# Kernel tuning notes

Measured on AMD Instinct MI355X. Metric: run time of the kernel, lower is better.

The kernel has to match this reference:

```python
import jax, jax.numpy as jnp
import numpy as np

# DualAttention dims
D_MODEL = 1024
H_SA = 8          # self-attention heads
H_RA = 8          # relational-attention heads
TOTAL_H = H_SA + H_RA
HEAD_DIM = D_MODEL // TOTAL_H   # 64
KEY_DIM = HEAD_DIM              # 64
N_REL = 8
REL_PROJ = HEAD_DIM * H_RA // N_REL  # 64
B, S = 2, 2048


def apply_rope(x, cos, sin):
    # x: [b, s, h, d]; cos/sin: [s, d//2]. Pairs are (0,1),(2,3),... as in
    # llama-style apply_rotary_emb (reshape(..., -1, 2).unbind(-1)).
    xr, xi = x[..., 0::2], x[..., 1::2]
    c = cos[None, :, None, :]
    s_ = sin[None, :, None, :]
    out = jnp.stack([xr * c - xi * s_, xr * s_ + xi * c], axis=-1)
    return out.reshape(x.shape)


def setup_inputs() -> dict:
    key = jax.random.key(0)
    ks = jax.random.split(key, 16)
    def w(k, shape):
        return jax.random.normal(k, shape, jnp.float32) * 0.02
    x = jax.random.normal(ks[0], (B, S, D_MODEL), jnp.float32)
    symbols = jax.random.normal(ks[1], (B, S, D_MODEL), jnp.float32)
    # real RoPE tables
    pos = np.arange(S, dtype=np.float32)[:, None]
    inv = 1.0 / (10000.0 ** (np.arange(0, KEY_DIM, 2, dtype=np.float32) / KEY_DIM))
    ang = pos * inv[None, :]
    freqs_cos = jnp.asarray(np.cos(ang), jnp.float32)
    freqs_sin = jnp.asarray(np.sin(ang), jnp.float32)
    return dict(
        x=x, symbols=symbols, freqs_cos=freqs_cos, freqs_sin=freqs_sin,
        # self-attention branch (torch Linear weights: [out, in])
        wq_sa=w(ks[2], (H_SA * KEY_DIM, D_MODEL)),
        wk_sa=w(ks[3], (H_SA * KEY_DIM, D_MODEL)),
        wv_sa=w(ks[4], (H_SA * HEAD_DIM, D_MODEL)),
        wo_sa=w(ks[5], (H_SA * HEAD_DIM, H_SA * HEAD_DIM)),
        # relational-attention branch
        wq_attn=w(ks[6], (H_RA * KEY_DIM, D_MODEL)),
        wk_attn=w(ks[7], (H_RA * KEY_DIM, D_MODEL)),
        wq_rel=w(ks[8], (N_REL * REL_PROJ, D_MODEL)),
        wk_rel=w(ks[9], (N_REL * REL_PROJ, D_MODEL)),
        wr=w(ks[10], (H_RA, HEAD_DIM, N_REL)),
        wv_ra=w(ks[11], (H_RA * HEAD_DIM, D_MODEL)),
        wo_ra=w(ks[12], (H_RA * HEAD_DIM, H_RA * HEAD_DIM)),
    )


def reference(x, symbols, freqs_cos, freqs_sin,
              wq_sa, wk_sa, wv_sa, wo_sa,
              wq_attn, wk_attn, wq_rel, wk_rel, wr, wv_ra, wo_ra):
    b, s, _ = x.shape
    attn_scale = 1.0 / np.sqrt(HEAD_DIM).astype(np.float32)
    rel_scale = 1.0 / np.sqrt(REL_PROJ).astype(np.float32)
    causal = jnp.tril(jnp.ones((s, s), dtype=bool))
    neg = jnp.finfo(x.dtype).min

    def heads(t, h, d):
        return t.reshape(b, s, h, d)

    # ---- self-attention branch (causal SDPA with RoPE) ----
    q = apply_rope(heads(x @ wq_sa.T, H_SA, KEY_DIM), freqs_cos, freqs_sin)
    k = apply_rope(heads(x @ wk_sa.T, H_SA, KEY_DIM), freqs_cos, freqs_sin)
    v = heads(x @ wv_sa.T, H_SA, HEAD_DIM)
    scores = jnp.einsum('bihd,bjhd->bhij', q, k) * attn_scale
    a = jax.nn.softmax(jnp.where(causal, scores, neg), axis=-1)
    sa_out = jnp.einsum('bhij,bjhd->bihd', a, v).reshape(b, s, H_SA * HEAD_DIM) @ wo_sa.T

    # ---- relational-attention branch ----
    # attention scores (softmax selection), with RoPE
    qa = apply_rope(heads(x @ wq_attn.T, H_RA, KEY_DIM), freqs_cos, freqs_sin)
    ka = apply_rope(heads(x @ wk_attn.T, H_RA, KEY_DIM), freqs_cos, freqs_sin)
    ra_scores = jnp.einsum('bihd,bjhd->bhij', qa, ka) * attn_scale
    alpha = jax.nn.softmax(jnp.where(causal, ra_scores, neg), axis=-1)
    # relations r(x_i, x_j) in R^{N_REL} (identity rel_activation)
    qr = heads(x @ wq_rel.T, N_REL, REL_PROJ)
    kr = heads(x @ wk_rel.T, N_REL, REL_PROJ)
    rel = jnp.einsum('birp,bjrp->brij', qr, kr) * rel_scale  # [b, R, i, j]
    # symbol values: wv applied to retrieved symbols
    sv = heads(symbols @ wv_ra.T, H_RA, HEAD_DIM)
    attended_sym = jnp.einsum('bhij,bjhd->bihd', alpha, sv)          # [b, i, h, d]
    attended_rel = jnp.einsum('bhij,brij->bihr', alpha, rel)         # [b, i, h, R]
    rel_out = jnp.einsum('bihr,hdr->bihd', attended_rel, wr)
    ra_out = (attended_sym + rel_out).reshape(b, s, H_RA * HEAD_DIM) @ wo_ra.T

    # DualAttention: concat branch outputs along feature dim -> [b, s, d_model]
    return jnp.concatenate([sa_out, ra_out], axis=-1)
```

## Files before the change

kernel.cpp:

```cpp
#include <hip/hip_runtime.h>

#define B_   2
#define S_   2048
#define H_   8
#define D_   64
#define DM_  1024
#define PJ_  512
#define NT_  32
#define NTRI 528
#define NCHK 80

typedef short bf16x8 __attribute__((ext_vector_type(8)));
typedef float f32x4 __attribute__((ext_vector_type(4)));

__device__ __forceinline__ float bf2f(unsigned int u) {
  return __uint_as_float(u << 16);
}
__device__ __forceinline__ unsigned short f2bf(float f) {
  unsigned int u = __float_as_uint(f);
  u += 0x7fffu + ((u >> 16) & 1u);
  return (unsigned short)(u >> 16);
}

__device__ __forceinline__ void glds16(const unsigned short* g, unsigned short* l) {
  __builtin_amdgcn_global_load_lds(
      (const __attribute__((address_space(1))) void*)g,
      (__attribute__((address_space(3))) void*)l, 16, 0, 0);
}

struct CvtJobs {
  const float*    src[12];
  unsigned short* dst[12];
  int             n4[12];
};

__global__ __launch_bounds__(256) void cvt_many(CvtJobs J) {
  const int j = blockIdx.y;
  const int i = blockIdx.x * 256 + threadIdx.x;
  if (i >= J.n4[j]) return;
  const float4 v = ((const float4*)J.src[j])[i];
  ushort4 o;
  o.x = f2bf(v.x); o.y = f2bf(v.y); o.z = f2bf(v.z); o.w = f2bf(v.w);
  ((ushort4*)J.dst[j])[i] = o;
}

__device__ __forceinline__
void gemm128_glds(const unsigned short* __restrict__ A, int m0,
                  const unsigned short* __restrict__ Wb,
                  unsigned short* __restrict__ Cb, int ldc, int KD,
                  unsigned short* As, unsigned short* Bs)
{
  const int tid = threadIdx.x;
  const int wv = tid >> 6, lane = tid & 63;
  const int r15 = lane & 15, quad = lane >> 4;
  const int wm = (wv >> 1) * 64, wn = (wv & 1) * 64;
  f32x4 acc[4][4];
#pragma unroll
  for (int i = 0; i < 4; ++i)
#pragma unroll
    for (int j = 0; j < 4; ++j) acc[i][j] = (f32x4){0.f, 0.f, 0.f, 0.f};

  const int srow = wv * 16 + (lane >> 2);
  const int scol = ((lane & 3) ^ ((lane >> 3) & 3)) * 8;
  const unsigned short* gaA0 = A + (size_t)(m0 + srow) * KD + scol;
  const unsigned short* gaA1 = gaA0 + (size_t)64 * KD;
  const unsigned short* gaB0 = Wb + (size_t)srow * KD + scol;
  const unsigned short* gaB1 = gaB0 + (size_t)64 * KD;
  unsigned short* ldsA0 = As + wv * 512;
  unsigned short* ldsA1 = As + 2048 + wv * 512;
  unsigned short* ldsB0 = Bs + wv * 512;
  unsigned short* ldsB1 = Bs + 2048 + wv * 512;
  const int rxor = (r15 >> 1) & 3;

  for (int kk = 0; kk < KD; kk += 32) {
    __syncthreads();
    glds16(gaA0 + kk, ldsA0);
    glds16(gaA1 + kk, ldsA1);
    glds16(gaB0 + kk, ldsB0);
    glds16(gaB1 + kk, ldsB1);
    __syncthreads();
    bf16x8 af[4], bf[4];
#pragma unroll
    for (int i = 0; i < 4; ++i)
      af[i] = *(const bf16x8*)(As + (wm + i * 16 + r15) * 32 + ((quad ^ rxor) << 3));
#pragma unroll
    for (int j = 0; j < 4; ++j)
      bf[j] = *(const bf16x8*)(Bs + (wn + j * 16 + r15) * 32 + ((quad ^ rxor) << 3));
#pragma unroll
    for (int i = 0; i < 4; ++i)
#pragma unroll
      for (int j = 0; j < 4; ++j)
        acc[i][j] = __builtin_amdgcn_mfma_f32_16x16x32_bf16(af[i], bf[j], acc[i][j], 0, 0, 0);
  }
#pragma unroll
  for (int i = 0; i < 4; ++i)
#pragma unroll
    for (int r = 0; r < 4; ++r) {
      unsigned short* cp = Cb + (size_t)(wm + i * 16 + quad * 4 + r) * ldc + wn + r15;
#pragma unroll
      for (int j = 0; j < 4; ++j) cp[j * 16] = f2bf(acc[i][j][r]);
    }
}

__global__ __launch_bounds__(256)
void proj_tiled(const unsigned short* __restrict__ XB,
                const unsigned short* __restrict__ SYB,
                const unsigned short* __restrict__ Wcat,
                unsigned short* __restrict__ Qbase,
                unsigned short* __restrict__ SV)
{
  __shared__ unsigned short As[128 * 32];
  __shared__ unsigned short Bs[128 * 32];
  const int m0 = blockIdx.x * 128;
  const int ny = blockIdx.y;
  const size_t NB = (size_t)B_ * S_ * PJ_;
  const unsigned short* A;
  const unsigned short* Wb;
  unsigned short* Cb;
  if (ny < 28) {
    const int n0 = ny * 128;
    A  = XB;
    Wb = Wcat + (size_t)n0 * DM_;
    Cb = Qbase + (size_t)(n0 >> 9) * NB + (size_t)m0 * PJ_ + (n0 & 511);
  } else {
    const int n0 = (ny - 28) * 128;
    A  = SYB;
    Wb = Wcat + (size_t)7 * PJ_ * DM_ + (size_t)n0 * DM_;
    Cb = SV + (size_t)m0 * PJ_ + n0;
  }
  gemm128_glds(A, m0, Wb, Cb, PJ_, DM_, As, Bs);
}

__global__ __launch_bounds__(256)
void out_tiled(const unsigned short* __restrict__ Asa,
               const unsigned short* __restrict__ Ara,
               const unsigned short* __restrict__ WOSA,
               const unsigned short* __restrict__ WORA,
               float* __restrict__ Out)
{
  __shared__ unsigned short As[128 * 40];
  __shared__ unsigned short Bs[64 * 40];
  const int m0 = blockIdx.x * 128;
  const int ny = blockIdx.y;
  const int n0 = (ny & 7) * 64;
  const unsigned short* A  = (ny < 8) ? Asa : Ara;
  const unsigned short* Wb = ((ny < 8) ? WOSA : WORA) + (size_t)n0 * PJ_;
  float* Cb = Out + (size_t)m0 * DM_ + ((ny < 8) ? 0 : 512) + n0;

  const int tid = threadIdx.x;
  const int wv = tid >> 6, lane = tid & 63;
  const int r15 = lane & 15, quad = lane >> 4;
  const int wm = wv * 32;
  f32x4 acc[2][4];
#pragma unroll
  for (int i = 0; i < 2; ++i)
#pragma unroll
    for (int j = 0; j < 4; ++j) acc[i][j] = (f32x4){0.f, 0.f, 0.f, 0.f};

  const int arow = tid >> 1, ac = (tid & 1) * 16;
  const int brow = tid >> 2, bc = (tid & 3) * 8;
  const unsigned short* ga = A + (size_t)(m0 + arow) * PJ_ + ac;
  const unsigned short* gb = Wb + (size_t)brow * PJ_ + bc;
  unsigned short* la = As + arow * 40 + ac;
  unsigned short* lb = Bs + brow * 40 + bc;

  for (int kk = 0; kk < PJ_; kk += 32) {
    __syncthreads();
    const uint4 a0 = *(const uint4*)(ga + kk);
    const uint4 a1 = *(const uint4*)(ga + kk + 8);
    const uint4 b0 = *(const uint4*)(gb + kk);
    *(uint4*)la       = a0;
    *(uint4*)(la + 8) = a1;
    *(uint4*)lb       = b0;
    __syncthreads();
    bf16x8 af[2], bf[4];
#pragma unroll
    for (int i = 0; i < 2; ++i)
      af[i] = *(const bf16x8*)(As + (wm + i * 16 + r15) * 40 + quad * 8);
#pragma unroll
    for (int j = 0; j < 4; ++j)
      bf[j] = *(const bf16x8*)(Bs + (j * 16 + r15) * 40 + quad * 8);
#pragma unroll
    for (int i = 0; i < 2; ++i)
#pragma unroll
      for (int j = 0; j < 4; ++j)
        acc[i][j] = __builtin_amdgcn_mfma_f32_16x16x32_bf16(af[i], bf[j], acc[i][j], 0, 0, 0);
  }
#pragma unroll
  for (int i = 0; i < 2; ++i)
#pragma unroll
    for (int r = 0; r < 4; ++r) {
      float* cp = Cb + (size_t)(wm + i * 16 + quad * 4 + r) * DM_ + r15;
#pragma unroll
      for (int j = 0; j < 4; ++j) cp[j * 16] = acc[i][j][r];
    }
}

__global__ __launch_bounds__(256)
void rel_rope(const unsigned short* __restrict__ QRg, const unsigned short* __restrict__ KRg,
              unsigned short* __restrict__ RelCF,
              unsigned short* __restrict__ Qp, unsigned short* __restrict__ Kp,
              unsigned short* __restrict__ QAp, unsigned short* __restrict__ KAp,
              const float* __restrict__ fcp, const float* __restrict__ fsp)
{
  __shared__ unsigned short As[128 * 72];
  __shared__ unsigned short Bs[128 * 72];
  const int t = blockIdx.x;
  int I = 0;
  while ((I + 1) * (I + 2) / 2 <= t) ++I;
  const int J = t - I * (I + 1) / 2;
  const int rr = blockIdx.y & 7, b = blockIdx.y >> 3;
  const int tid = threadIdx.x;
  const int wv = tid >> 6, lane = tid & 63;
  const int r15 = lane & 15, quad = lane >> 4;

  const int srow = tid >> 1, c32 = (tid & 1) * 32;
  const unsigned short* ga = QRg + (size_t)(b * S_ + I * 128 + srow) * PJ_ + rr * 64 + c32;
  const unsigned short* gb = KRg + (size_t)(b * S_ + J * 128 + srow) * PJ_ + rr * 64 + c32;
  unsigned short* la = As + srow * 72 + c32;
  unsigned short* lb = Bs + srow * 72 + c32;
#pragma unroll
  for (int q = 0; q < 4; ++q) {
    *(uint4*)(la + q * 8) = *(const uint4*)(ga + q * 8);
    *(uint4*)(lb + q * 8) = *(const uint4*)(gb + q * 8);
  }
  __syncthreads();

  const int wm = (wv >> 1) * 64, wn = (wv & 1) * 64;
  const int it64 = 2 * I + (wv >> 1), jt64 = 2 * J + (wv & 1);
  if (jt64 <= it64) {
    f32x4 acc[4][4];
#pragma unroll
    for (int a = 0; a < 4; ++a)
#pragma unroll
      for (int bq = 0; bq < 4; ++bq) acc[a][bq] = (f32x4){0.f, 0.f, 0.f, 0.f};
#pragma unroll
    for (int k0 = 0; k0 < 2; ++k0) {
      bf16x8 af[4], bf[4];
#pragma unroll
      for (int i = 0; i < 4; ++i)
        af[i] = *(const bf16x8*)(As + (wm + i * 16 + r15) * 72 + quad * 8 + k0 * 32);
#pragma unroll
      for (int j = 0; j < 4; ++j)
        bf[j] = *(const bf16x8*)(Bs + (wn + j * 16 + r15) * 72 + quad * 8 + k0 * 32);
#pragma unroll
      for (int a = 0; a < 4; ++a)
#pragma unroll
        for (int bq = 0; bq < 4; ++bq)
          acc[a][bq] = __builtin_amdgcn_mfma_f32_16x16x32_bf16(bf[a], af[bq], acc[a][bq], 0, 0, 0);
    }
    unsigned short* out = RelCF + ((size_t)(b * 8 + rr) * NTRI + (size_t)it64 * (it64 + 1) / 2 + jt64) * 4096;
#pragma unroll
    for (int bq = 0; bq < 4; ++bq) {
      unsigned short tmp[16];
#pragma unroll
      for (int a = 0; a < 4; ++a)
#pragma unroll
        for (int r = 0; r < 4; ++r)
          tmp[a * 4 + r] = f2bf(acc[a][bq][r] * 0.125f);
      unsigned short* op = out + (size_t)(bq * 64 + lane) * 16;
      *(uint4*)op       = *(const uint4*)tmp;
      *(uint4*)(op + 8) = *(const uint4*)(tmp + 8);
    }
  }

  const int bid = (int)blockIdx.y * 136 + (int)blockIdx.x;
  const int gt = bid * 256 + tid;
#pragma unroll
  for (int k = 0; k < 2; ++k) {
    const int i = gt * 2 + k;
    if (i >= 4 * 262144) continue;
    const int tn = i >> 18;
    const int r2 = i & 262143;
    unsigned short* P = (tn == 0) ? Qp : (tn == 1) ? Kp : (tn == 2) ? QAp : KAp;
    const int b2 = r2 >> 17;
    const int s2 = (r2 >> 6) & 2047;
    const int c8 = (r2 & 63) * 8;
    const int ci0 = (c8 & 63) >> 1;
    const size_t off2 = ((size_t)(b2 * S_ + s2)) * PJ_ + c8;
    uint4 v = *(const uint4*)(P + off2);
    unsigned int u[4] = {v.x, v.y, v.z, v.w};
    unsigned int o[4];
#pragma unroll
    for (int q = 0; q < 4; ++q) {
      const float xr = __uint_as_float(u[q] << 16);
      const float xi = __uint_as_float(u[q] & 0xffff0000u);
      const float cs = fcp[s2 * 32 + ci0 + q];
      const float sn = fsp[s2 * 32 + ci0 + q];
      const unsigned short lo = f2bf(xr * cs - xi * sn);
      const unsigned short hi = f2bf(xr * sn + xi * cs);
      o[q] = (unsigned int)lo | ((unsigned int)hi << 16);
    }
    uint4 ov; ov.x = o[0]; ov.y = o[1]; ov.z = o[2]; ov.w = o[3];
    *(uint4*)(P + off2) = ov;
  }
}

__global__ __launch_bounds__(256)
void flash_part(const unsigned short* __restrict__ Qsa, const unsigned short* __restrict__ Ksa,
                const unsigned short* __restrict__ Vsa,
                const unsigned short* __restrict__ Qra, const unsigned short* __restrict__ Kra,
                const unsigned short* __restrict__ SVra,
                const unsigned short* __restrict__ RelCF,
                unsigned short* __restrict__ PoP, float* __restrict__ lP,
                float* __restrict__ arpP)
{
  __shared__ unsigned short Ks[2][64][72];
  __shared__ unsigned short Vt[2][64][72];
  const int x = blockIdx.x;
  int it, c;
  if (x < 8)       { it = x;                    c = 0; }
  else if (x < 24) { it = 8 + ((x - 8) >> 1);   c = (x - 8) & 1; }
  else if (x < 48) { it = 16 + (x - 24) / 3;    c = (x - 24) % 3; }
  else             { it = 24 + ((x - 48) >> 2); c = (x - 48) & 3; }
  const int j0 = c * 8;
  const int jend = (j0 + 8 < it + 1) ? (j0 + 8) : (it + 1);
  const bool ra = (blockIdx.y >= 8);
  const int h = blockIdx.y & 7;
  const int b = blockIdx.z;
  const int chunkId = (b * 16 + (int)blockIdx.y) * NCHK + x;
  const unsigned short* Qg = ra ? Qra : Qsa;
  const unsigned short* Kg = ra ? Kra : Ksa;
  const unsigned short* Vg = ra ? SVra : Vsa;
  const int tid = threadIdx.x;
  const int wv = tid >> 6, lane = tid & 63;
  const int r15 = lane & 15, quad = lane >> 4;
  const size_t bh = (size_t)b * S_ * PJ_ + (size_t)h * D_;
  const size_t relStride = (size_t)NTRI * 4096;

  const int kr0 = tid >> 3, kc0 = (tid & 7) << 3;
  const int kr1 = (tid + 256) >> 3;
  const unsigned short* kgp = Kg + bh + kc0;
  const unsigned short* vgp = Vg + bh + (size_t)lane * PJ_ + wv * 8;
  const int kcol = ((lane >> 2) & 3) * 8 + ((lane >> 4) & 1) * 4 + (lane & 3) + (lane >> 5) * 32;

  const unsigned short* qp = Qg + bh + (size_t)(it * 64 + wv * 16 + r15) * PJ_ + quad * 8;
  const bf16x8 aq0 = *(const bf16x8*)qp;
  const bf16x8 aq1 = *(const bf16x8*)(qp + 32);

  f32x4 o_acc[4];
  float l_row = 0.f;
  float arp[8];
#pragma unroll
  for (int n = 0; n < 4; ++n) o_acc[n] = (f32x4){0.f, 0.f, 0.f, 0.f};
#pragma unroll
  for (int rr = 0; rr < 8; ++rr) arp[rr] = 0.f;
  const int il = wv * 16 + r15;
  const size_t relTileBase = (size_t)(b * 8) * NTRI * 4096
                           + (size_t)(it * (it + 1)) / 2 * 4096
                           + (size_t)(wv * 64 + lane) * 16;

  uint4 ka0, ka1, va0, va1;
  {
    const size_t jb = (size_t)j0 * 64 * PJ_;
    ka0 = *(const uint4*)(kgp + jb + (size_t)kr0 * PJ_);
    ka1 = *(const uint4*)(kgp + jb + (size_t)kr1 * PJ_);
    va0 = *(const uint4*)(vgp + jb);
    va1 = *(const uint4*)(vgp + jb + 32);
  }
  int p = 0;
  {
    *(uint4*)&Ks[0][kr0][kc0] = ka0;
    *(uint4*)&Ks[0][kr1][kc0] = ka1;
    unsigned short t8[8];
    *(uint4*)t8 = va0;
#pragma unroll
    for (int m = 0; m < 8; ++m) Vt[0][wv * 8 + m][kcol] = t8[m];
    *(uint4*)t8 = va1;
#pragma unroll
    for (int m = 0; m < 8; ++m) Vt[0][wv * 8 + 32 + m][kcol] = t8[m];
  }
  __syncthreads();

  for (int jt = j0; jt < jend; ++jt) {
    const bool more = (jt + 1 < jend);
    if (more) {
      const size_t jb = (size_t)(jt + 1) * 64 * PJ_;
      ka0 = *(const uint4*)(kgp + jb + (size_t)kr0 * PJ_);
      ka1 = *(const uint4*)(kgp + jb + (size_t)kr1 * PJ_);
      va0 = *(const uint4*)(vgp + jb);
      va1 = *(const uint4*)(vgp + jb + 32);
    }
    uint4 pre[8];
    const unsigned short* rtBase = RelCF + relTileBase + (size_t)jt * 4096;
    if (ra) {
      const unsigned short* rt = rtBase;
#pragma unroll
      for (int q = 0; q < 4; ++q) {
        pre[2 * q]     = *(const uint4*)rt;
        pre[2 * q + 1] = *(const uint4*)(rt + 8);
        rt += relStride;
      }
    }
    f32x4 s[4];
#pragma unroll
    for (int n = 0; n < 4; ++n) s[n] = (f32x4){0.f, 0.f, 0.f, 0.f};
#pragma unroll
    for (int k0 = 0; k0 < 2; ++k0) {
      const bf16x8 bq = k0 ? aq1 : aq0;
#pragma unroll
      for (int n = 0; n < 4; ++n) {
        const bf16x8 kf = *(const bf16x8*)&Ks[p][n * 16 + r15][quad * 8 + k0 * 32];
        s[n] = __builtin_amdgcn_mfma_f32_16x16x32_bf16(kf, bq, s[n], 0, 0, 0);
      }
    }
    if (jt == it) {
#pragma unroll
      for (int n = 0; n < 4; ++n)
#pragma unroll
        for (int r = 0; r < 4; ++r) {
          const bool ok = (n * 16 + quad * 4 + r <= il);
          s[n][r] = ok ? __expf(s[n][r] * 0.125f - 4.0f) : 0.f;
        }
    } else {
#pragma unroll
      for (int n = 0; n < 4; ++n)
#pragma unroll
        for (int r = 0; r < 4; ++r)
          s[n][r] = __expf(s[n][r] * 0.125f - 4.0f);
    }
    unsigned short pw[16];
#pragma unroll
    for (int jj = 0; jj < 8; ++jj) {
      pw[jj]     = f2bf(s[(jj >> 2)][jj & 3]);
      pw[8 + jj] = f2bf(s[2 + (jj >> 2)][jj & 3]);
    }
    const bf16x8 pa0 = *(const bf16x8*)pw;
    const bf16x8 pa1 = *(const bf16x8*)(pw + 8);
    {
      float ls = 0.f;
#pragma unroll
      for (int jj = 0; jj < 16; ++jj) ls += bf2f((unsigned int)pw[jj]);
      l_row += ls;
    }
#pragma unroll
    for (int k0 = 0; k0 < 2; ++k0) {
      const bf16x8 pf = k0 ? pa1 : pa0;
#pragma unroll
      for (int n = 0; n < 4; ++n) {
        const bf16x8 vf = *(const bf16x8*)&Vt[p][n * 16 + r15][quad * 8 + k0 * 32];
        o_acc[n] = __builtin_amdgcn_mfma_f32_16x16x32_bf16(pf, vf, o_acc[n], 0, 0, 0);
      }
    }
    if (ra) {
      const unsigned short* rt2 = rtBase + 4 * relStride;
#pragma unroll
      for (int rr = 0; rr < 8; ++rr) {
        unsigned int ru[8];
        if (rr < 4) {
          *(uint4*)ru       = pre[2 * rr];
          *(uint4*)(ru + 4) = pre[2 * rr + 1];
        } else {
          *(uint4*)ru       = *(const uint4*)rt2;
          *(uint4*)(ru + 4) = *(const uint4*)(rt2 + 8);
          rt2 += relStride;
        }
        float a = arp[rr];
#pragma unroll
        for (int n = 0; n < 4; ++n) {
          const unsigned int u0 = ru[2 * n], u1 = ru[2 * n + 1];
          a += s[n][0] * __uint_as_float(u0 << 16);
          a += s[n][1] * __uint_as_float(u0 & 0xffff0000u);
          a += s[n][2] * __uint_as_float(u1 << 16);
          a += s[n][3] * __uint_as_float(u1 & 0xffff0000u);
        }
        arp[rr] = a;
      }
    }
    if (more) {
      const int q = p ^ 1;
      *(uint4*)&Ks[q][kr0][kc0] = ka0;
      *(uint4*)&Ks[q][kr1][kc0] = ka1;
      unsigned short t8[8];
      *(uint4*)t8 = va0;
#pragma unroll
      for (int m = 0; m < 8; ++m) Vt[q][wv * 8 + m][kcol] = t8[m];
      *(uint4*)t8 = va1;
#pragma unroll
      for (int m = 0; m < 8; ++m) Vt[q][wv * 8 + 32 + m][kcol] = t8[m];
      __syncthreads();
      p = q;
    }
  }
  unsigned short* po = PoP + (size_t)chunkId * 4096;
#pragma unroll
  for (int n = 0; n < 4; ++n)
#pragma unroll
    for (int r = 0; r < 4; ++r)
      po[(wv * 16 + quad * 4 + r) * 64 + n * 16 + r15] = f2bf(o_acc[n][r]);
  l_row += __shfl_xor(l_row, 16);
  l_row += __shfl_xor(l_row, 32);
  if (lane < 16)
    lP[(size_t)chunkId * 64 + wv * 16 + lane] = l_row;
  if (ra) {
#pragma unroll
    for (int rr = 0; rr < 8; ++rr) {
      arp[rr] += __shfl_xor(arp[rr], 16);
      arp[rr] += __shfl_xor(arp[rr], 32);
    }
    if (lane < 16) {
      float* ap = arpP + (size_t)chunkId * 512 + (wv * 16 + lane) * 8;
#pragma unroll
      for (int rr = 0; rr < 8; ++rr) ap[rr] = arp[rr];
    }
  }
}

__global__ __launch_bounds__(256)
void flash_merge(const unsigned short* __restrict__ PoP, const float* __restrict__ lP,
                 const float* __restrict__ arpP, const float* __restrict__ wrF,
                 unsigned short* __restrict__ Osa, unsigned short* __restrict__ Ora)
{
  const int it = blockIdx.x;
  const int hh = blockIdx.y;
  const int b  = blockIdx.z;
  const bool ra = (hh >= 8);
  const int h = hh & 7;
  const int nc = it / 8 + 1;
  int cb;
  if (it < 8)       cb = it;
  else if (it < 16) cb = 8 + 2 * (it - 8);
  else if (it < 24) cb = 24 + 3 * (it - 16);
  else              cb = 48 + 4 * (it - 24);
  const int cid0 = (b * 16 + hh) * NCHK + cb;
  const int tid = threadIdx.x;
  const int row = tid >> 2;
  const int cg  = tid & 3;

  float L = 0.f;
  for (int c = 0; c < nc; ++c) L += lP[(size_t)(cid0 + c) * 64 + row];
  const float inv = 1.f / L;

  float o[16];
#pragma unroll
  for (int k = 0; k < 16; ++k) o[k] = 0.f;
  for (int c = 0; c < nc; ++c) {
    const unsigned short* pp = PoP + (size_t)(cid0 + c) * 4096 + row * 64 + cg * 16;
    unsigned int u[8];
    *(uint4*)u       = *(const uint4*)pp;
    *(uint4*)(u + 4) = *(const uint4*)(pp + 8);
#pragma unroll
    for (int q = 0; q < 8; ++q) {
      o[2 * q]     += __uint_as_float(u[q] << 16);
      o[2 * q + 1] += __uint_as_float(u[q] & 0xffff0000u);
    }
  }
  if (ra) {
    float A[8];
#pragma unroll
    for (int rr = 0; rr < 8; ++rr) A[rr] = 0.f;
    for (int c = 0; c < nc; ++c) {
      const float* ap = arpP + (size_t)(cid0 + c) * 512 + row * 8;
#pragma unroll
      for (int rr = 0; rr < 8; ++rr) A[rr] += ap[rr];
    }
#pragma unroll
    for (int k = 0; k < 16; ++k) {
      const float* wp = wrF + ((size_t)h * 64 + cg * 16 + k) * 8;
      float ro = 0.f;
#pragma unroll
      for (int rr = 0; rr < 8; ++rr) ro += A[rr] * wp[rr];
      o[k] += ro;
    }
  }
  const size_t bh = (size_t)b * S_ * PJ_ + (size_t)h * D_;
  unsigned short* op = (ra ? Ora : Osa) + bh + (size_t)(it * 64 + row) * PJ_ + cg * 16;
#pragma unroll
  for (int k = 0; k < 16; ++k) op[k] = f2bf(o[k] * inv);
}

extern "C" void kernel_launch(void* const* d_in, const int* in_sizes, int n_in,
                              void* d_out, int out_size, void* d_ws, size_t ws_size,
                              hipStream_t stream)
{
  (void)in_sizes; (void)n_in; (void)out_size; (void)ws_size;
  const float* x    = (const float*)d_in[0];
  const float* sym  = (const float*)d_in[1];
  const float* fc   = (const float*)d_in[2];
  const float* fs   = (const float*)d_in[3];
  const float* wqsa = (const float*)d_in[4];
  const float* wksa = (const float*)d_in[5];
  const float* wvsa = (const float*)d_in[6];
  const float* wosa = (const float*)d_in[7];
  const float* wqat = (const float*)d_in[8];
  const float* wkat = (const float*)d_in[9];
  const float* wqre = (const float*)d_in[10];
  const float* wkre = (const float*)d_in[11];
  const float* wr   = (const float*)d_in[12];
  const float* wvra = (const float*)d_in[13];
  const float* wora = (const float*)d_in[14];

  unsigned short* wsb = (unsigned short*)d_ws;
  const size_t NX = (size_t)B_ * S_ * DM_;
  const size_t NB = (size_t)B_ * S_ * PJ_;
  const size_t NW = (size_t)PJ_ * DM_;
  const size_t NO = (size_t)PJ_ * PJ_;
  const size_t NR = (size_t)B_ * 8 * NTRI * 4096;
  const size_t NCH = (size_t)B_ * 16 * NCHK;

  size_t off = 0;
  unsigned short* XB   = wsb + off; off += NX;
  unsigned short* SYB  = wsb + off; off += NX;
  unsigned short* WB[8];
  for (int i = 0; i < 8; ++i) { WB[i] = wsb + off; off += NW; }
  unsigned short* WOSA = wsb + off; off += NO;
  unsigned short* WORA = wsb + off; off += NO;
  unsigned short* Q    = wsb + off; off += NB;
  unsigned short* K    = wsb + off; off += NB;
  unsigned short* V    = wsb + off; off += NB;
  unsigned short* QA   = wsb + off; off += NB;
  unsigned short* KA   = wsb + off; off += NB;
  unsigned short* QR   = wsb + off; off += NB;
  unsigned short* KR   = wsb + off; off += NB;
  unsigned short* SV   = wsb + off; off += NB;
  unsigned short* Asa  = wsb + off; off += NB;
  unsigned short* Ara  = wsb + off; off += NB;
  unsigned short* RelCF = wsb + off; off += NR;
  unsigned short* PoP  = XB;
  float* lP   = (float*)(wsb + off); off += NCH * 64 * 2;
  float* arpP = (float*)(wsb + off); off += NCH * 512 * 2;

  CvtJobs cj;
  cj.src[0]  = x;    cj.dst[0]  = XB;    cj.n4[0]  = (int)(NX / 4);
  cj.src[1]  = sym;  cj.dst[1]  = SYB;   cj.n4[1]  = (int)(NX / 4);
  cj.src[2]  = wqsa; cj.dst[2]  = WB[0]; cj.n4[2]  = (int)(NW / 4);
  cj.src[3]  = wksa; cj.dst[3]  = WB[1]; cj.n4[3]  = (int)(NW / 4);
  cj.src[4]  = wvsa; cj.dst[4]  = WB[2]; cj.n4[4]  = (int)(NW / 4);
  cj.src[5]  = wqat; cj.dst[5]  = WB[3]; cj.n4[5]  = (int)(NW / 4);
  cj.src[6]  = wkat; cj.dst[6]  = WB[4]; cj.n4[6]  = (int)(NW / 4);
  cj.src[7]  = wqre; cj.dst[7]  = WB[5]; cj.n4[7]  = (int)(NW / 4);
  cj.src[8]  = wkre; cj.dst[8]  = WB[6]; cj.n4[8]  = (int)(NW / 4);
  cj.src[9]  = wvra; cj.dst[9]  = WB[7]; cj.n4[9]  = (int)(NW / 4);
  cj.src[10] = wosa; cj.dst[10] = WOSA;  cj.n4[10] = (int)(NO / 4);
  cj.src[11] = wora; cj.dst[11] = WORA;  cj.n4[11] = (int)(NO / 4);
  cvt_many<<<dim3(4096, 12), dim3(256), 0, stream>>>(cj);

  proj_tiled<<<dim3(32, 32), dim3(256), 0, stream>>>(XB, SYB, WB[0], Q, SV);
  rel_rope<<<dim3(136, 16), dim3(256), 0, stream>>>(QR, KR, RelCF, Q, K, QA, KA, fc, fs);
  flash_part<<<dim3(NCHK, 16, B_), dim3(256), 0, stream>>>(
      Q, K, V, QA, KA, SV, RelCF, PoP, lP, arpP);
  flash_merge<<<dim3(NT_, 16, B_), dim3(256), 0, stream>>>(
      PoP, lP, arpP, wr, Asa, Ara);
  out_tiled<<<dim3(32, 16), dim3(256), 0, stream>>>(Asa, Ara, WOSA, WORA, (float*)d_out);
}
```

Baseline: 317.4 us.

## Move relation and row-sum reductions in flash_part onto MFMA

The per-lane scalar FMA loops that accumulated alpha-weighted relation values are replaced with MFMA products of the bf16 probability fragments against relation tiles. This requires changing the RelCF tile layout written by the producer kernel. Row sums now come from an MFMA against a ones vector, and exp uses a folded exp2 with a packed bf16 conversion instruction. Block order is reversed so the long causal chunks start first. The aim is to cut VALU work in the attention inner loop, at the cost of extra MFMA issue slots and only the diagonal relation entries being used.

```diff
diff --git a/kernel.cpp b/kernel.cpp
--- a/kernel.cpp
+++ b/kernel.cpp
@@ -20,6 +20,14 @@
   unsigned int u = __float_as_uint(f);
   u += 0x7fffu + ((u >> 16) & 1u);
   return (unsigned short)(u >> 16);
+}
+__device__ __forceinline__ unsigned int cvtpk_bf16(float lo, float hi) {
+  unsigned int r;
+  asm("v_cvt_pk_bf16_f32 %0, %1, %2" : "=v"(r) : "v"(lo), "v"(hi));
+  return r;
+}
+__device__ __forceinline__ bf16x8 u4_to_bf(uint4 v) {
+  union { uint4 a; bf16x8 b; } u; u.a = v; return u.b;
 }
 
 __device__ __forceinline__ void glds16(const unsigned short* g, unsigned short* l) {
@@ -258,9 +266,9 @@
 #pragma unroll
         for (int r = 0; r < 4; ++r)
           tmp[a * 4 + r] = f2bf(acc[a][bq][r] * 0.125f);
-      unsigned short* op = out + (size_t)(bq * 64 + lane) * 16;
-      *(uint4*)op       = *(const uint4*)tmp;
-      *(uint4*)(op + 8) = *(const uint4*)(tmp + 8);
+      unsigned short* op = out + (size_t)bq * 1024 + (size_t)lane * 8;
+      *(uint4*)op         = *(const uint4*)tmp;
+      *(uint4*)(op + 512) = *(const uint4*)(tmp + 8);
     }
   }
 
@@ -307,7 +315,7 @@
 {
   __shared__ unsigned short Ks[2][64][72];
   __shared__ unsigned short Vt[2][64][72];
-  const int x = blockIdx.x;
+  const int x = NCHK - 1 - (int)blockIdx.x;
   int it, c;
   if (x < 8)       { it = x;                    c = 0; }
   else if (x < 24) { it = 8 + ((x - 8) >> 1);   c = (x - 8) & 1; }
@@ -338,17 +346,19 @@
   const bf16x8 aq0 = *(const bf16x8*)qp;
   const bf16x8 aq1 = *(const bf16x8*)(qp + 32);
 
+  const bf16x8 ones = (bf16x8)(short)0x3F80;
+
   f32x4 o_acc[4];
-  float l_row = 0.f;
-  float arp[8];
+  f32x4 l_acc = (f32x4){0.f, 0.f, 0.f, 0.f};
+  f32x4 accR[8];
 #pragma unroll
   for (int n = 0; n < 4; ++n) o_acc[n] = (f32x4){0.f, 0.f, 0.f, 0.f};
 #pragma unroll
-  for (int rr = 0; rr < 8; ++rr) arp[rr] = 0.f;
+  for (int rr = 0; rr < 8; ++rr) accR[rr] = (f32x4){0.f, 0.f, 0.f, 0.f};
   const int il = wv * 16 + r15;
   const size_t relTileBase = (size_t)(b * 8) * NTRI * 4096
                            + (size_t)(it * (it + 1)) / 2 * 4096
-                           + (size_t)(wv * 64 + lane) * 16;
+                           + (size_t)wv * 1024 + (size_t)lane * 8;
 
   uint4 ka0, ka1, va0, va1;
   {
@@ -388,7 +398,7 @@
 #pragma unroll
       for (int q = 0; q < 4; ++q) {
         pre[2 * q]     = *(const uint4*)rt;
-        pre[2 * q + 1] = *(const uint4*)(rt + 8);
+        pre[2 * q + 1] = *(const uint4*)(rt + 512);
         rt += relStride;
       }
     }
@@ -410,28 +420,30 @@
 #pragma unroll
         for (int r = 0; r < 4; ++r) {
           const bool ok = (n * 16 + quad * 4 + r <= il);
-          s[n][r] = ok ? __expf(s[n][r] * 0.125f - 4.0f) : 0.f;
+          s[n][r] = ok ? exp2f(fmaf(s[n][r], 0.180336887f, -5.770780163f)) : 0.f;
         }
     } else {
 #pragma unroll
       for (int n = 0; n < 4; ++n)
 #pragma unroll
         for (int r = 0; r < 4; ++r)
-          s[n][r] = __expf(s[n][r] * 0.125f - 4.0f);
-    }
-    unsigned short pw[16];
-#pragma unroll
-    for (int jj = 0; jj < 8; ++jj) {
-      pw[jj]     = f2bf(s[(jj >> 2)][jj & 3]);
-      pw[8 + jj] = f2bf(s[2 + (jj >> 2)][jj & 3]);
-    }
-    const bf16x8 pa0 = *(const bf16x8*)pw;
-    const bf16x8 pa1 = *(const bf16x8*)(pw + 8);
-    {
-      float ls = 0.f;
-#pragma unroll
-      for (int jj = 0; jj < 16; ++jj) ls += bf2f((unsigned int)pw[jj]);
-      l_row += ls;
+          s[n][r] = exp2f(fmaf(s[n][r], 0.180336887f, -5.770780163f));
+    }
+    uint4 w0, w1;
+    w0.x = cvtpk_bf16(s[0][0], s[0][1]); w0.y = cvtpk_bf16(s[0][2], s[0][3]);
+    w0.z = cvtpk_bf16(s[1][0], s[1][1]); w0.w = cvtpk_bf16(s[1][2], s[1][3]);
+    w1.x = cvtpk_bf16(s[2][0], s[2][1]); w1.y = cvtpk_bf16(s[2][2], s[2][3]);
+    w1.z = cvtpk_bf16(s[3][0], s[3][1]); w1.w = cvtpk_bf16(s[3][2], s[3][3]);
+    const bf16x8 pa0 = u4_to_bf(w0);
+    const bf16x8 pa1 = u4_to_bf(w1);
+    l_acc = __builtin_amdgcn_mfma_f32_16x16x32_bf16(pa0, ones, l_acc, 0, 0, 0);
+    l_acc = __builtin_amdgcn_mfma_f32_16x16x32_bf16(pa1, ones, l_acc, 0, 0, 0);
+    if (ra) {
+#pragma unroll
+      for (int rr = 0; rr < 4; ++rr) {
+        accR[rr] = __builtin_amdgcn_mfma_f32_16x16x32_bf16(pa0, u4_to_bf(pre[2 * rr]), accR[rr], 0, 0, 0);
+        accR[rr] = __builtin_amdgcn_mfma_f32_16x16x32_bf16(pa1, u4_to_bf(pre[2 * rr + 1]), accR[rr], 0, 0, 0);
+      }
     }
 #pragma unroll
     for (int k0 = 0; k0 < 2; ++k0) {
@@ -445,26 +457,12 @@
     if (ra) {
       const unsigned short* rt2 = rtBase + 4 * relStride;
 #pragma unroll
-      for (int rr = 0; rr < 8; ++rr) {
-        unsigned int ru[8];
-        if (rr < 4) {
-          *(uint4*)ru       = pre[2 * rr];
-          *(uint4*)(ru + 4) = pre[2 * rr + 1];
-        } else {
-          *(uint4*)ru       = *(const uint4*)rt2;
-          *(uint4*)(ru + 4) = *(const uint4*)(rt2 + 8);
-          rt2 += relStride;
-        }
-        float a = arp[rr];
-#pragma unroll
-        for (int n = 0; n < 4; ++n) {
-          const unsigned int u0 = ru[2 * n], u1 = ru[2 * n + 1];
-          a += s[n][0] * __uint_as_float(u0 << 16);
-          a += s[n][1] * __uint_as_float(u0 & 0xffff0000u);
-          a += s[n][2] * __uint_as_float(u1 << 16);
-          a += s[n][3] * __uint_as_float(u1 & 0xffff0000u);
-        }
-        arp[rr] = a;
+      for (int rr = 4; rr < 8; ++rr) {
+        const bf16x8 rb0 = *(const bf16x8*)rt2;
+        const bf16x8 rb1 = *(const bf16x8*)(rt2 + 512);
+        accR[rr] = __builtin_amdgcn_mfma_f32_16x16x32_bf16(pa0, rb0, accR[rr], 0, 0, 0);
+        accR[rr] = __builtin_amdgcn_mfma_f32_16x16x32_bf16(pa1, rb1, accR[rr], 0, 0, 0);
+        rt2 += relStride;
       }
     }
     if (more) {
@@ -488,20 +486,19 @@
 #pragma unroll
     for (int r = 0; r < 4; ++r)
       po[(wv * 16 + quad * 4 + r) * 64 + n * 16 + r15] = f2bf(o_acc[n][r]);
-  l_row += __shfl_xor(l_row, 16);
-  l_row += __shfl_xor(l_row, 32);
-  if (lane < 16)
-    lP[(size_t)chunkId * 64 + wv * 16 + lane] = l_row;
-  if (ra) {
+  if (r15 == 0) {
+#pragma unroll
+    for (int r = 0; r < 4; ++r)
+      lP[(size_t)chunkId * 64 + wv * 16 + quad * 4 + r] = l_acc[r];
+  }
+  if (ra && quad == (r15 >> 2)) {
+    const int d3 = r15 & 3;
+    float* ap = arpP + (size_t)chunkId * 512 + (size_t)(wv * 16 + r15) * 8;
 #pragma unroll
     for (int rr = 0; rr < 8; ++rr) {
-      arp[rr] += __shfl_xor(arp[rr], 16);
-      arp[rr] += __shfl_xor(arp[rr], 32);
-    }
-    if (lane < 16) {
-      float* ap = arpP + (size_t)chunkId * 512 + (wv * 16 + lane) * 8;
-#pragma unroll
-      for (int rr = 0; rr < 8; ++rr) ap[rr] = arp[rr];
+      const f32x4 a4 = accR[rr];
+      const float v = (d3 == 0) ? a4[0] : (d3 == 1) ? a4[1] : (d3 == 2) ? a4[2] : a4[3];
+      ap[rr] = v;
     }
   }
 }
```

Measured after the change: 317.7 us. No clear change (+0.1%).
